# Kernel optimization log

Measured on AMD Instinct MI355X. Metric: run time of the kernel, lower is better.

## Reference

```python
import jax, jax.numpy as jnp
import numpy as np
from jax import lax

L, B, C, H, NUM_LAYERS = 512, 64, 1024, 1024, 2


def setup_inputs() -> dict:
    key = jax.random.key(0)
    ks = jax.random.split(key, 8)
    scale = 0.05
    inp = {
        "x": jax.random.normal(ks[0], (L, B, C), dtype=jnp.float32),
        "W_ih0": jax.random.normal(ks[1], (4 * H, C), dtype=jnp.float32) * scale,
        "W_hh0": jax.random.normal(ks[2], (4 * H, H), dtype=jnp.float32) * scale,
        "b0": jnp.zeros((4 * H,), dtype=jnp.float32),
        "W_ih1": jax.random.normal(ks[3], (4 * H, H), dtype=jnp.float32) * scale,
        "W_hh1": jax.random.normal(ks[4], (4 * H, H), dtype=jnp.float32) * scale,
        "b1": jnp.zeros((4 * H,), dtype=jnp.float32),
    }
    return inp


def _lstm_layer(x_seq, W_ih, W_hh, b):
    # x_seq: [L, B, in]; W_ih: [4H, in]; W_hh: [4H, H]; b: [4H]
    # Precompute the input-side GEMM for the whole sequence (same math as
    # the per-step torch Linear, just batched over t).
    xg = jnp.einsum('tbc,gc->tbg', x_seq, W_ih) + b  # [L, B, 4H]
    Bsz = x_seq.shape[1]
    Hh = W_hh.shape[1]
    h0 = jnp.zeros((Bsz, Hh), dtype=x_seq.dtype)
    c0 = jnp.zeros((Bsz, Hh), dtype=x_seq.dtype)

    def step(carry, xg_t):
        h, c = carry
        gates = xg_t + h @ W_hh.T  # [B, 4H]
        i, f, g, o = jnp.split(gates, 4, axis=1)
        i = jax.nn.sigmoid(i)
        f = jax.nn.sigmoid(f)
        g = jnp.tanh(g)
        o = jax.nn.sigmoid(o)
        # NOTE: faithful to the source — h uses the PREVIOUS cell state c,
        # then c is updated (the source computes h before updating c).
        h_new = o * jnp.tanh(c)
        c_new = f * c + i * g
        return (h_new, c_new), h_new

    (h_n, c_n), ys = lax.scan(step, (h0, c0), xg)
    return ys, h_n, c_n


def reference(x, W_ih0, W_hh0, b0, W_ih1, W_hh1, b1):
    y0, h0n, c0n = _lstm_layer(x, W_ih0, W_hh0, b0)
    y1, h1n, c1n = _lstm_layer(y0, W_ih1, W_hh1, b1)
    h_n = jnp.stack([h0n, h1n], axis=0)  # [num_layers, B, H]
    c_n = jnp.stack([c0n, c1n], axis=0)
    return y1, h_n, c_n
```

## Files before the change

### kernel.cpp

```cpp
#include <hip/hip_runtime.h>

typedef _Float16 half8 __attribute__((ext_vector_type(8)));
typedef float f32x16 __attribute__((ext_vector_type(16)));
typedef unsigned long long u64;

#define SEQ 512
#define HID 1024
#define HB 65536

#define WROW 2064
#define LDS_WIH 0
#define LDS_WHH 66048
#define LDS_GX0 132096
#define LDS_GX1 141312
#define LDS_GH  150528
#define LDS_ARR 159744
#define LDS_TOTAL 159808

__device__ __forceinline__ float sigf(float x) { return 1.0f / (1.0f + __expf(-x)); }
__device__ __forceinline__ float tanhfast(float x) {
  x = fminf(fmaxf(x, -44.0f), 44.0f);
  float e = __expf(2.0f * x);
  return (e - 1.0f) / (e + 1.0f);
}

__global__ __launch_bounds__(256, 1) void cvt_blk(const float* __restrict__ in,
                                                  _Float16* __restrict__ out, int nItems) {
  int stride = gridDim.x * blockDim.x;
  for (int g = blockIdx.x * blockDim.x + threadIdx.x; g < nItems; g += stride) {
    int t = g >> 13;
    int r = g & 8191;
    int kc = r >> 6;
    int b = r & 63;
    const float* sp = in + (((size_t)t * 64 + b) << 10) + kc * 8;
    float4 v0 = *(const float4*)sp;
    float4 v1 = *(const float4*)(sp + 4);
    half8 o;
    o[0] = (_Float16)v0.x; o[1] = (_Float16)v0.y; o[2] = (_Float16)v0.z; o[3] = (_Float16)v0.w;
    o[4] = (_Float16)v1.x; o[5] = (_Float16)v1.y; o[6] = (_Float16)v1.z; o[7] = (_Float16)v1.w;
    ((half8*)out)[g] = o;
  }
}

__device__ __forceinline__ void pollFlags(const unsigned* f, unsigned tgt, int lane) {
  const u64* fp = (const u64*)f;
  for (;;) {
    u64 v = __hip_atomic_load(fp + lane, __ATOMIC_RELAXED, __HIP_MEMORY_SCOPE_AGENT);
    unsigned a = (unsigned)v, b = (unsigned)(v >> 32);
    unsigned mn = a < b ? a : b;
    if (__all(mn >= tgt)) break;
    __builtin_amdgcn_s_sleep(1);
  }
}

__device__ __forceinline__ f32x16 gemm_k(const _Float16* aPtr, const char* wB, int bsub) {
  f32x16 acc[4];
#pragma unroll
  for (int q = 0; q < 4; ++q)
#pragma unroll
    for (int i = 0; i < 16; ++i) acc[q][i] = 0.0f;

  half8 aw[4][8];
  half8 bw[2][8];
#pragma unroll
  for (int w0 = 0; w0 < 3; ++w0)
#pragma unroll
    for (int u = 0; u < 8; ++u) aw[w0][u] = *(const half8*)(aPtr + (w0 * 8 + u) * 1024);
#pragma unroll
  for (int u = 0; u < 8; ++u) bw[0][u] = *(const half8*)(wB + u * 32 + bsub);

#pragma unroll
  for (int w = 0; w < 8; ++w) {
    if (w + 3 < 8) {
#pragma unroll
      for (int u = 0; u < 8; ++u)
        aw[(w + 3) & 3][u] = *(const half8*)(aPtr + ((w + 3) * 8 + u) * 1024);
    }
    if (w + 1 < 8) {
#pragma unroll
      for (int u = 0; u < 8; ++u)
        bw[(w + 1) & 1][u] = *(const half8*)(wB + ((w + 1) * 8 + u) * 32 + bsub);
    }
#pragma unroll
    for (int u = 0; u < 8; ++u)
      acc[u & 3] = __builtin_amdgcn_mfma_f32_32x32x16_f16(aw[w & 3][u], bw[w & 1][u],
                                                          acc[u & 3], 0, 0, 0);
  }
  return acc[0] + acc[1] + acc[2] + acc[3];
}

__device__ __forceinline__ void writeGates(float* gbuf, const f32x16& t, int mtile, int lane) {
#pragma unroll
  for (int r = 0; r < 16; ++r) {
    int bl = (r & 3) + ((r >> 2) << 3) + ((lane >> 5) << 2);
    gbuf[(mtile * 32 + bl) * 36 + (lane & 31)] = t[r];
  }
}

__global__ __launch_bounds__(256, 1) void lstm_fused(
    const _Float16* __restrict__ xh,
    const float* __restrict__ Wih0, const float* __restrict__ Whh0, const float* __restrict__ b0,
    const float* __restrict__ Wih1, const float* __restrict__ Whh1, const float* __restrict__ b1,
    _Float16* __restrict__ h0buf, _Float16* __restrict__ h1buf,
    unsigned* __restrict__ flags, float* __restrict__ out) {
  extern __shared__ char smem[];
  float* gH = (float*)(smem + LDS_GH);
  unsigned* arrCnt = (unsigned*)(smem + LDS_ARR);

  const int tid = threadIdx.x;
  const int lane = tid & 63;
  const int wave = tid >> 6;
  const int mtile = wave & 1;
  const int gsel = wave >> 1;
  const int wg = blockIdx.x;
  const int layer = wg >> 7;
  const int lw = wg & 127;
  const int j0 = lw * 8;

  const float* wsrc0 = layer ? Wih1 : Wih0;
  const float* wsrc1 = layer ? Whh1 : Whh0;
  for (int m = 0; m < 2; ++m) {
    const float* src = m ? wsrc1 : wsrc0;
    char* base = smem + (m ? LDS_WHH : LDS_WIH);
    for (int q = tid; q < 4096; q += 256) {
      int r = q >> 7;
      int kc = (q & 127) << 3;
      int grow = ((r >> 3) << 10) + j0 + (r & 7);
      const float* sp = src + (size_t)grow * 1024 + kc;
      half8 v;
#pragma unroll
      for (int j = 0; j < 8; ++j) v[j] = (_Float16)sp[j];
      *(half8*)(base + r * WROW + kc * 2) = v;
    }
  }
  const float* bsrc = layer ? b1 : b0;
  const int jmy = tid & 7;
  const float bi_r = bsrc[j0 + jmy];
  const float bf_r = bsrc[1024 + j0 + jmy];
  const float bg_r = bsrc[2048 + j0 + jmy];
  const float bo_r = bsrc[3072 + j0 + jmy];
  float creg[2] = {0.0f, 0.0f};
  if (tid == 0) *arrCnt = 0u;
  __syncthreads();

  const int arow = mtile * 32 + (lane & 31);
  const int aoff = ((lane >> 5) << 9) + arow * 8;
  const int brow = lane & 31;
  const int bsub = (lane >> 5) << 4;
  const char* wIH = smem + LDS_WIH + brow * WROW;
  const char* wHH = smem + LDS_WHH + brow * WROW;
  _Float16* hSelf = layer ? h1buf : h0buf;
  const unsigned* flagsSelf = flags + (layer << 7);
  float* outy = out;
  float* outh = out + 33554432;
  float* outc = out + 33685504;

  if (gsel == 0) {
    if (layer) pollFlags(flags, 1u, lane);
    const _Float16* aB = layer ? (h0buf + (size_t)1 * HB) : xh;
    f32x16 t = gemm_k(aB + aoff, wIH, bsub);
    writeGates((float*)(smem + LDS_GX0), t, mtile, lane);
  }

  for (int k = 0; k < SEQ; ++k) {
    __syncthreads();
    if (gsel == 0) {
      if (k + 1 < SEQ) {
        if (layer) pollFlags(flags, (unsigned)(k + 2), lane);
        const _Float16* aB =
            layer ? (h0buf + (size_t)(k + 2) * HB) : (xh + (size_t)(k + 1) * HB);
        f32x16 t = gemm_k(aB + aoff, wIH, bsub);
        writeGates((float*)(smem + ((k + 1) & 1 ? LDS_GX1 : LDS_GX0)), t, mtile, lane);
      }
    } else {
      if (k > 0) pollFlags(flagsSelf, (unsigned)k, lane);
      f32x16 t = gemm_k(hSelf + (size_t)k * HB + aoff, wHH, bsub);
      writeGates(gH, t, mtile, lane);
    }
    __syncthreads();

    const float* gX = (const float*)(smem + ((k & 1) ? LDS_GX1 : LDS_GX0));
    u64* hw64 = (u64*)(hSelf + (size_t)(k + 1) * HB);
    const bool last = (k == SEQ - 1);
    float hnv[2], cnv[2];
#pragma unroll
    for (int it = 0; it < 2; ++it) {
      int item = tid + it * 256;
      int b = item >> 3, j = item & 7;
      float vi = gX[b * 36 + j] + gH[b * 36 + j] + bi_r;
      float vf = gX[b * 36 + 8 + j] + gH[b * 36 + 8 + j] + bf_r;
      float vg = gX[b * 36 + 16 + j] + gH[b * 36 + 16 + j] + bg_r;
      float vo = gX[b * 36 + 24 + j] + gH[b * 36 + 24 + j] + bo_r;
      float i_ = sigf(vi), f_ = sigf(vf), g_ = tanhfast(vg), o_ = sigf(vo);
      float cp = creg[it];
      float hn = o_ * tanhfast(cp);
      float cn = f_ * cp + i_ * g_;
      creg[it] = cn;
      hnv[it] = hn; cnv[it] = cn;
      union { _Float16 h; unsigned short u; } hb; hb.h = (_Float16)hn;
      unsigned lo = (unsigned)hb.u;
      unsigned pr1 = (unsigned)__shfl_xor((int)lo, 1, 64);
      unsigned pk32 = lo | (pr1 << 16);
      u64 pr2 = (u64)(unsigned)__shfl_xor((int)pk32, 2, 64);
      if ((j & 3) == 0) {
        u64 v = (u64)pk32 | (pr2 << 32);
        __hip_atomic_store(hw64 + (lw * 64 + b) * 2 + (j >> 2), v, __ATOMIC_RELAXED,
                           __HIP_MEMORY_SCOPE_AGENT);
      }
    }
    asm volatile("s_waitcnt vmcnt(0)" ::: "memory");
    if (lane == 0) {
      unsigned old = atomicAdd(arrCnt, 1u);
      if (old == 4u * (unsigned)k + 3u)
        __hip_atomic_store(&flags[wg], (unsigned)(k + 1), __ATOMIC_RELAXED,
                           __HIP_MEMORY_SCOPE_AGENT);
    }
#pragma unroll
    for (int it = 0; it < 2; ++it) {
      int item = tid + it * 256;
      int b = item >> 3, j = item & 7;
      int col = j0 + j;
      if (layer)
        __builtin_nontemporal_store(hnv[it], &outy[(size_t)k * HB + b * HID + col]);
      if (last) {
        __builtin_nontemporal_store(hnv[it], &outh[layer * HB + b * HID + col]);
        __builtin_nontemporal_store(cnv[it], &outc[layer * HB + b * HID + col]);
      }
    }
  }
}

extern "C" void kernel_launch(void* const* d_in, const int* in_sizes, int n_in,
                              void* d_out, int out_size, void* d_ws, size_t ws_size,
                              hipStream_t stream) {
  const float* x = (const float*)d_in[0];
  const float* Wih0 = (const float*)d_in[1];
  const float* Whh0 = (const float*)d_in[2];
  const float* b0 = (const float*)d_in[3];
  const float* Wih1 = (const float*)d_in[4];
  const float* Whh1 = (const float*)d_in[5];
  const float* b1 = (const float*)d_in[6];
  float* out = (float*)d_out;

  char* ws = (char*)d_ws;
  _Float16* xh = (_Float16*)ws;
  _Float16* h0 = (_Float16*)(ws + 67108864);
  _Float16* h1 = (_Float16*)(ws + 134348800);
  unsigned* flags = (unsigned*)(ws + 201588736);

  hipMemsetAsync(h0, 0, 131072, stream);
  hipMemsetAsync(h1, 0, 131072, stream);
  hipMemsetAsync(flags, 0, 1024, stream);
  cvt_blk<<<4096, 256, 0, stream>>>(x, xh, 512 * 128 * 64);
  lstm_fused<<<256, 256, LDS_TOTAL, stream>>>(xh, Wih0, Whh0, b0, Wih1, Whh1, b1,
                                              h0, h1, flags, out);
}
```

Baseline: 2.990 ms.

## Split recurrent GEMM K dimension across all four waves with LDS atomic accumulation

Previously two waves ran the input-projection GEMM for the next step while two waves ran the recurrent W_hh GEMM over the full K. Now all four waves split K in half for both GEMMs and accumulate into a single LDS gate buffer with atomicAdd. The buffer is zeroed after the gates are read. The next step's input GEMM now runs after the cell update rather than overlapping the recurrent GEMM. The aim is to halve the latency of the recurrent GEMM on the serial critical path, at the cost of LDS atomics, an extra barrier, and losing the earlier overlap.

Result: slower. 7.312 ms (+144.5%).

```diff
diff --git a/kernel.cpp b/kernel.cpp
--- a/kernel.cpp
+++ b/kernel.cpp
@@ -11,11 +11,9 @@
 #define WROW 2064
 #define LDS_WIH 0
 #define LDS_WHH 66048
-#define LDS_GX0 132096
-#define LDS_GX1 141312
-#define LDS_GH  150528
-#define LDS_ARR 159744
-#define LDS_TOTAL 159808
+#define LDS_GX  132096
+#define LDS_ARR 141312
+#define LDS_TOTAL 141376
 
 __device__ __forceinline__ float sigf(float x) { return 1.0f / (1.0f + __expf(-x)); }
 __device__ __forceinline__ float tanhfast(float x) {
@@ -53,6 +51,7 @@
   }
 }
 
+template <int NW>
 __device__ __forceinline__ f32x16 gemm_k(const _Float16* aPtr, const char* wB, int bsub) {
   f32x16 acc[4];
 #pragma unroll
@@ -63,20 +62,20 @@
   half8 aw[4][8];
   half8 bw[2][8];
 #pragma unroll
-  for (int w0 = 0; w0 < 3; ++w0)
+  for (int w0 = 0; w0 < (NW < 3 ? NW : 3); ++w0)
 #pragma unroll
     for (int u = 0; u < 8; ++u) aw[w0][u] = *(const half8*)(aPtr + (w0 * 8 + u) * 1024);
 #pragma unroll
   for (int u = 0; u < 8; ++u) bw[0][u] = *(const half8*)(wB + u * 32 + bsub);
 
 #pragma unroll
-  for (int w = 0; w < 8; ++w) {
-    if (w + 3 < 8) {
+  for (int w = 0; w < NW; ++w) {
+    if (w + 3 < NW) {
 #pragma unroll
       for (int u = 0; u < 8; ++u)
         aw[(w + 3) & 3][u] = *(const half8*)(aPtr + ((w + 3) * 8 + u) * 1024);
     }
-    if (w + 1 < 8) {
+    if (w + 1 < NW) {
 #pragma unroll
       for (int u = 0; u < 8; ++u)
         bw[(w + 1) & 1][u] = *(const half8*)(wB + ((w + 1) * 8 + u) * 32 + bsub);
@@ -89,11 +88,11 @@
   return acc[0] + acc[1] + acc[2] + acc[3];
 }
 
-__device__ __forceinline__ void writeGates(float* gbuf, const f32x16& t, int mtile, int lane) {
+__device__ __forceinline__ void addGates(float* gbuf, const f32x16& t, int mtile, int lane) {
 #pragma unroll
   for (int r = 0; r < 16; ++r) {
     int bl = (r & 3) + ((r >> 2) << 3) + ((lane >> 5) << 2);
-    gbuf[(mtile * 32 + bl) * 36 + (lane & 31)] = t[r];
+    atomicAdd(&gbuf[(mtile * 32 + bl) * 36 + (lane & 31)], t[r]);
   }
 }
 
@@ -104,14 +103,14 @@
     _Float16* __restrict__ h0buf, _Float16* __restrict__ h1buf,
     unsigned* __restrict__ flags, float* __restrict__ out) {
   extern __shared__ char smem[];
-  float* gH = (float*)(smem + LDS_GH);
+  float* gX = (float*)(smem + LDS_GX);
   unsigned* arrCnt = (unsigned*)(smem + LDS_ARR);
 
   const int tid = threadIdx.x;
   const int lane = tid & 63;
   const int wave = tid >> 6;
   const int mtile = wave & 1;
-  const int gsel = wave >> 1;
+  const int khalf = wave >> 1;
   const int wg = blockIdx.x;
   const int layer = wg >> 7;
   const int lw = wg & 127;
@@ -140,46 +139,37 @@
   const float bg_r = bsrc[2048 + j0 + jmy];
   const float bo_r = bsrc[3072 + j0 + jmy];
   float creg[2] = {0.0f, 0.0f};
+  for (int q = tid; q < 64 * 36; q += 256) gX[q] = 0.0f;
   if (tid == 0) *arrCnt = 0u;
   __syncthreads();
 
   const int arow = mtile * 32 + (lane & 31);
-  const int aoff = ((lane >> 5) << 9) + arow * 8;
+  const int aoffR = khalf * 32768 + ((lane >> 5) << 9) + arow * 8;
   const int brow = lane & 31;
   const int bsub = (lane >> 5) << 4;
-  const char* wIH = smem + LDS_WIH + brow * WROW;
-  const char* wHH = smem + LDS_WHH + brow * WROW;
+  const char* wIH = smem + LDS_WIH + brow * WROW + khalf * 1024;
+  const char* wHH = smem + LDS_WHH + brow * WROW + khalf * 1024;
   _Float16* hSelf = layer ? h1buf : h0buf;
   const unsigned* flagsSelf = flags + (layer << 7);
   float* outy = out;
   float* outh = out + 33554432;
   float* outc = out + 33685504;
 
-  if (gsel == 0) {
+  {
     if (layer) pollFlags(flags, 1u, lane);
     const _Float16* aB = layer ? (h0buf + (size_t)1 * HB) : xh;
-    f32x16 t = gemm_k(aB + aoff, wIH, bsub);
-    writeGates((float*)(smem + LDS_GX0), t, mtile, lane);
+    f32x16 t = gemm_k<4>(aB + aoffR, wIH, bsub);
+    addGates(gX, t, mtile, lane);
   }
 
   for (int k = 0; k < SEQ; ++k) {
+    if (k > 0) pollFlags(flagsSelf, (unsigned)k, lane);
+    {
+      f32x16 t = gemm_k<4>(hSelf + (size_t)k * HB + aoffR, wHH, bsub);
+      addGates(gX, t, mtile, lane);
+    }
     __syncthreads();
-    if (gsel == 0) {
-      if (k + 1 < SEQ) {
-        if (layer) pollFlags(flags, (unsigned)(k + 2), lane);
-        const _Float16* aB =
-            layer ? (h0buf + (size_t)(k + 2) * HB) : (xh + (size_t)(k + 1) * HB);
-        f32x16 t = gemm_k(aB + aoff, wIH, bsub);
-        writeGates((float*)(smem + ((k + 1) & 1 ? LDS_GX1 : LDS_GX0)), t, mtile, lane);
-      }
-    } else {
-      if (k > 0) pollFlags(flagsSelf, (unsigned)k, lane);
-      f32x16 t = gemm_k(hSelf + (size_t)k * HB + aoff, wHH, bsub);
-      writeGates(gH, t, mtile, lane);
-    }
-    __syncthreads();
-
-    const float* gX = (const float*)(smem + ((k & 1) ? LDS_GX1 : LDS_GX0));
+
     u64* hw64 = (u64*)(hSelf + (size_t)(k + 1) * HB);
     const bool last = (k == SEQ - 1);
     float hnv[2], cnv[2];
@@ -187,10 +177,14 @@
     for (int it = 0; it < 2; ++it) {
       int item = tid + it * 256;
       int b = item >> 3, j = item & 7;
-      float vi = gX[b * 36 + j] + gH[b * 36 + j] + bi_r;
-      float vf = gX[b * 36 + 8 + j] + gH[b * 36 + 8 + j] + bf_r;
-      float vg = gX[b * 36 + 16 + j] + gH[b * 36 + 16 + j] + bg_r;
-      float vo = gX[b * 36 + 24 + j] + gH[b * 36 + 24 + j] + bo_r;
+      float vi = gX[b * 36 + j] + bi_r;
+      float vf = gX[b * 36 + 8 + j] + bf_r;
+      float vg = gX[b * 36 + 16 + j] + bg_r;
+      float vo = gX[b * 36 + 24 + j] + bo_r;
+      gX[b * 36 + j] = 0.0f;
+      gX[b * 36 + 8 + j] = 0.0f;
+      gX[b * 36 + 16 + j] = 0.0f;
+      gX[b * 36 + 24 + j] = 0.0f;
       float i_ = sigf(vi), f_ = sigf(vf), g_ = tanhfast(vg), o_ = sigf(vo);
       float cp = creg[it];
       float hn = o_ * tanhfast(cp);
@@ -227,6 +221,15 @@
         __builtin_nontemporal_store(cnv[it], &outc[layer * HB + b * HID + col]);
       }
     }
+    __syncthreads();
+
+    if (k + 1 < SEQ) {
+      if (layer) pollFlags(flags, (unsigned)(k + 2), lane);
+      const _Float16* aB =
+          layer ? (h0buf + (size_t)(k + 2) * HB) : (xh + (size_t)(k + 1) * HB);
+      f32x16 t = gemm_k<4>(aB + aoffR, wIH, bsub);
+      addGates(gX, t, mtile, lane);
+    }
   }
 }
 
```
